# Optimization experiments

Hardware: AMD Instinct MI355X
Metric: run time of the kernel (lower is better)

## Reference

```python
import jax, jax.numpy as jnp
import numpy as np

D = 1024      # features
C = 768       # context dim
H = 16        # heads
HD = D // H   # head dim = 64
N = 2048      # query tokens
M = 2048      # context tokens
EPS = 1e-12
SCALE = float(np.sqrt(HD))


def layernorm(x, w, b):
    c = x - x.mean(axis=-1, keepdims=True)
    s = (c * c).mean(axis=-1, keepdims=True)
    return c * jax.lax.rsqrt(s + EPS) * w + b


def setup_inputs() -> dict:
    key = jax.random.key(0)
    ks = jax.random.split(key, 10)
    sc = 0.02
    return {
        "x": jax.random.normal(ks[0], (N, D), jnp.float32),
        "ctx": jax.random.normal(ks[1], (M, C), jnp.float32),
        # attention projections (Projection: normal*0.02, zero bias)
        "wq": jax.random.normal(ks[2], (D, D), jnp.float32) * sc,
        "bq": jnp.zeros((D,), jnp.float32),
        "wk": jax.random.normal(ks[3], (C, D), jnp.float32) * sc,
        "bk": jnp.zeros((D,), jnp.float32),
        "wv": jax.random.normal(ks[4], (C, D), jnp.float32) * sc,
        "bv": jnp.zeros((D,), jnp.float32),
        "wo": jax.random.normal(ks[5], (D, D), jnp.float32) * sc,
        "bo": jnp.zeros((D,), jnp.float32),
        # MLP
        "w1": jax.random.normal(ks[6], (D, 4 * D), jnp.float32) * sc,
        "b1": jnp.zeros((4 * D,), jnp.float32),
        "w2": jax.random.normal(ks[7], (4 * D, D), jnp.float32) * sc,
        "b2": jnp.zeros((D,), jnp.float32),
        # layernorms
        "qn_w": jnp.ones((D,), jnp.float32), "qn_b": jnp.zeros((D,), jnp.float32),
        "kvn_w": jnp.ones((C,), jnp.float32), "kvn_b": jnp.zeros((C,), jnp.float32),
        "pn_w": jnp.ones((D,), jnp.float32), "pn_b": jnp.zeros((D,), jnp.float32),
    }


def reference(x, ctx, wq, bq, wk, bk, wv, bv, wo, bo, w1, b1, w2, b2,
              qn_w, qn_b, kvn_w, kvn_b, pn_w, pn_b):
    # pre-norm cross-attention
    xq = layernorm(x, qn_w, qn_b)          # [n, d]
    kv = layernorm(ctx, kvn_w, kvn_b)      # [m, c]
    q = (xq @ wq + bq).reshape(N, H, HD).transpose(1, 0, 2)   # [h, n, hd]
    k = (kv @ wk + bk).reshape(M, H, HD).transpose(1, 0, 2)   # [h, m, hd]
    v = (kv @ wv + bv).reshape(M, H, HD).transpose(1, 0, 2)   # [h, m, hd]
    attn = jax.nn.softmax(jnp.einsum('hnd,hmd->hnm', q, k) / SCALE, axis=-1)
    o = jnp.einsum('hnm,hmd->hnd', attn, v).transpose(1, 0, 2).reshape(N, D)
    x = (o @ wo + bo) + x
    # MLP block
    h = layernorm(x, pn_w, pn_b)
    h = jax.nn.gelu(h @ w1 + b1) @ w2 + b2
    return h + x
```

## Files before the change

### kernel.cpp

```cpp
#include <hip/hip_runtime.h>

typedef __bf16 bf16;
typedef __bf16 bf16x4 __attribute__((ext_vector_type(4)));
typedef __bf16 bf16x8 __attribute__((ext_vector_type(8)));
typedef float f32x4 __attribute__((ext_vector_type(4)));

#define N_TOK 2048
#define M_TOK 2048
#define DIM 1024
#define CDIM 768
#define DFF 4096

static __device__ __forceinline__ void async16(const void* g, void* l) {
  __builtin_amdgcn_global_load_lds((const __attribute__((address_space(1))) void*)g,
                                   (__attribute__((address_space(3))) void*)l, 16, 0, 0);
}

__global__ __launch_bounds__(256) void detect_kernel(const void* x, int* flag) {
  __shared__ int cnt;
  if (threadIdx.x == 0) cnt = 0;
  __syncthreads();
  const unsigned* w = (const unsigned*)x;
  int ok = 0;
  for (int i = threadIdx.x; i < 512; i += 256) {
    unsigned lo = w[i] & 0xFFFFu;
    float f = __uint_as_float(lo << 16);
    if (lo == 0u || (fabsf(f) > 1e-3f && fabsf(f) < 1e3f)) ok++;
  }
  atomicAdd(&cnt, ok);
  __syncthreads();
  if (threadIdx.x == 0) *flag = (cnt >= 256) ? 1 : 0;
}

struct ConvArgs {
  const void* src[12];
  bf16* dst[12];
  int n[12];
};
__global__ __launch_bounds__(256) void conv_small_kernel(ConvArgs a, const int* flag) {
  const bool isbf = (*flag != 0);
  const int b = blockIdx.x;
  const void* in = a.src[b];
  bf16* out = a.dst[b];
  const int n = a.n[b];
  for (int i = threadIdx.x; i < n; i += 256)
    out[i] = isbf ? ((const bf16*)in)[i] : (bf16)((const float*)in)[i];
}

struct TmArgs {
  const void* src[4];
  bf16* dst[4];
  int r0[4], Rcnt[4], c0[4], Cfull[4], gx[4], gy[4];
  int force_bf;
};
__global__ __launch_bounds__(256) void tmulti_kernel(TmArgs a, const int* flag) {
  const int z = blockIdx.z;
  if ((int)blockIdx.x >= a.gx[z] || (int)blockIdx.y >= a.gy[z]) return;
  __shared__ bf16 t[32][33];
  const bool isbf = a.force_bf || (*flag != 0);
  const void* in = a.src[z];
  bf16* out = a.dst[z];
  const int Rcnt = a.Rcnt[z], Cfull = a.Cfull[z];
  const int cb = blockIdx.x * 32, rb = blockIdx.y * 32;
  const int tx = threadIdx.x & 31, ty = threadIdx.x >> 5;
#pragma unroll
  for (int i = 0; i < 4; i++) {
    const size_t r = (size_t)(a.r0[z] + rb + ty + i * 8);
    const size_t c = (size_t)(a.c0[z] + cb + tx);
    float v = isbf ? (float)((const bf16*)in)[r * Cfull + c]
                   : ((const float*)in)[r * Cfull + c];
    t[ty + i * 8][tx] = (bf16)v;
  }
  __syncthreads();
#pragma unroll
  for (int i = 0; i < 4; i++)
    out[(size_t)(cb + ty + i * 8) * Rcnt + rb + tx] = t[tx][ty + i * 8];
}

__global__ __launch_bounds__(256) void ln_pair_kernel(
    const void* __restrict__ x0, const bf16* w0, const bf16* b0, bf16* o0,
    const void* __restrict__ x1, const bf16* w1, const bf16* b1, bf16* o1,
    const int* flag) {
  const bool isbf = (*flag != 0);
  const int cols = (blockIdx.y == 0) ? DIM : CDIM;
  const void* x = (blockIdx.y == 0) ? x0 : x1;
  const bf16* w = (blockIdx.y == 0) ? w0 : w1;
  const bf16* b = (blockIdx.y == 0) ? b0 : b1;
  bf16* outp = (blockIdx.y == 0) ? o0 : o1;
  const int row = blockIdx.x;
  const bf16* xr_b = (const bf16*)x + (size_t)row * cols;
  const float* xr_f = (const float*)x + (size_t)row * cols;
  bf16* orow = outp + (size_t)row * cols;
  float s = 0.f, ss = 0.f;
  for (int c = threadIdx.x; c < cols; c += 256) {
    float v = isbf ? (float)xr_b[c] : xr_f[c];
    s += v; ss += v * v;
  }
  for (int d = 1; d < 64; d <<= 1) { s += __shfl_xor(s, d, 64); ss += __shfl_xor(ss, d, 64); }
  __shared__ float sh[8];
  const int wv = threadIdx.x >> 6, lane = threadIdx.x & 63;
  if (lane == 0) { sh[wv] = s; sh[4 + wv] = ss; }
  __syncthreads();
  s = sh[0] + sh[1] + sh[2] + sh[3];
  ss = sh[4] + sh[5] + sh[6] + sh[7];
  const float mean = s / cols;
  float var = ss / cols - mean * mean;
  var = fmaxf(var, 0.f);
  const float r = rsqrtf(var + 1e-12f);
  for (int c = threadIdx.x; c < cols; c += 256) {
    float v = isbf ? (float)xr_b[c] : xr_f[c];
    orow[c] = (bf16)((v - mean) * r * (float)w[c] + (float)b[c]);
  }
}

__global__ __launch_bounds__(256) void ln_kernel(
    const bf16* __restrict__ x, const bf16* __restrict__ w, const bf16* __restrict__ b,
    bf16* __restrict__ out, int cols) {
  const int row = blockIdx.x;
  const bf16* xr = x + (size_t)row * cols;
  bf16* orow = out + (size_t)row * cols;
  float s = 0.f, ss = 0.f;
  for (int c = threadIdx.x; c < cols; c += 256) {
    float v = (float)xr[c];
    s += v; ss += v * v;
  }
  for (int d = 1; d < 64; d <<= 1) { s += __shfl_xor(s, d, 64); ss += __shfl_xor(ss, d, 64); }
  __shared__ float sh[8];
  const int wv = threadIdx.x >> 6, lane = threadIdx.x & 63;
  if (lane == 0) { sh[wv] = s; sh[4 + wv] = ss; }
  __syncthreads();
  s = sh[0] + sh[1] + sh[2] + sh[3];
  ss = sh[4] + sh[5] + sh[6] + sh[7];
  const float mean = s / cols;
  float var = ss / cols - mean * mean;
  var = fmaxf(var, 0.f);
  const float r = rsqrtf(var + 1e-12f);
  for (int c = threadIdx.x; c < cols; c += 256) {
    float v = (float)xr[c];
    orow[c] = (bf16)((v - mean) * r * (float)w[c] + (float)b[c]);
  }
}

__device__ __forceinline__ float gelu_f(float x) {
  float u = 0.7978845608028654f * (x + 0.044715f * x * x * x);
  return 0.5f * x * (1.f + tanhf(u));
}

template <int EPI>
__global__ __launch_bounds__(256) void gemm64(
    const bf16* __restrict__ A, const bf16* __restrict__ Bt,
    const bf16* __restrict__ bias, const void* __restrict__ resid,
    void* __restrict__ Cout, int K, int ldc, const int* flag) {
  __shared__ __align__(16) bf16 As[2][64 * 32];
  __shared__ __align__(16) bf16 Bs[2][64 * 32];
  const int tid = threadIdx.x;
  const int lane = tid & 63, wv = tid >> 6;
  const int lq = lane >> 4, lm = lane & 15;
  const int row0 = blockIdx.y * 64, col0 = blockIdx.x * 64;
  const int wr = (wv >> 1) * 32, wc = (wv & 1) * 32;

  f32x4 acc[2][2] = {};
  const int r_a = wv * 16 + (lane >> 2);
  const int kc = (lane & 3) * 8;

  for (int k0 = 0; k0 < K; k0 += 64) {
    __syncthreads();
#pragma unroll
    for (int b = 0; b < 2; b++) {
      async16(A + (size_t)(row0 + r_a) * K + k0 + b * 32 + kc, As[b] + wv * 512);
      async16(Bt + (size_t)(col0 + r_a) * K + k0 + b * 32 + kc, Bs[b] + wv * 512);
    }
    __syncthreads();
#pragma unroll
    for (int b = 0; b < 2; b++) {
      bf16x8 af[2], bfv[2];
#pragma unroll
      for (int t = 0; t < 2; t++)
        af[t] = *(const bf16x8*)&As[b][(wr + t * 16 + lm) * 32 + lq * 8];
#pragma unroll
      for (int t = 0; t < 2; t++)
        bfv[t] = *(const bf16x8*)&Bs[b][(wc + t * 16 + lm) * 32 + lq * 8];
#pragma unroll
      for (int i = 0; i < 2; i++)
#pragma unroll
        for (int j = 0; j < 2; j++)
          acc[i][j] = __builtin_amdgcn_mfma_f32_16x16x32_bf16(af[i], bfv[j], acc[i][j], 0, 0, 0);
    }
  }

  const bool isbf = (*flag != 0);
#pragma unroll
  for (int i = 0; i < 2; i++) {
    const int rb = row0 + wr + i * 16 + lq * 4;
#pragma unroll
    for (int j = 0; j < 2; j++) {
      const int c = col0 + wc + j * 16 + lm;
      const float bv = (EPI != 5) ? (float)bias[c] : 0.f;
#pragma unroll
      for (int rg = 0; rg < 4; rg++) {
        const size_t idx = (size_t)(rb + rg) * ldc + c;
        float v = acc[i][j][rg] + bv;
        if (EPI == 1)
          v += isbf ? (float)((const bf16*)resid)[idx] : ((const float*)resid)[idx];
        if (EPI == 2) v = gelu_f(v);
        if (EPI == 4) v += (float)((const bf16*)resid)[idx];
        if (EPI == 5)
          v += isbf ? (float)((bf16*)Cout)[idx] : ((float*)Cout)[idx];
        if (EPI == 4 || EPI == 5) {
          if (isbf) ((bf16*)Cout)[idx] = (bf16)v;
          else      ((float*)Cout)[idx] = v;
        } else {
          ((bf16*)Cout)[idx] = (bf16)v;
        }
      }
    }
  }
}

struct QkvArgs {
  const bf16* A[3];
  const bf16* Bt[3];
  const bf16* bias[3];
  bf16* C[3];
  int K[3], ldc[3], gx[3], gy[3], brow[3];
};
__global__ __launch_bounds__(256) void gemm64_qkv(QkvArgs a) {
  const int z = blockIdx.z;
  if ((int)blockIdx.x >= a.gx[z] || (int)blockIdx.y >= a.gy[z]) return;
  const bf16* A = a.A[z];
  const bf16* Bt = a.Bt[z];
  const int K = a.K[z];
  __shared__ __align__(16) bf16 As[2][64 * 32];
  __shared__ __align__(16) bf16 Bs[2][64 * 32];
  const int tid = threadIdx.x;
  const int lane = tid & 63, wv = tid >> 6;
  const int lq = lane >> 4, lm = lane & 15;
  const int row0 = blockIdx.y * 64, col0 = blockIdx.x * 64;
  const int wr = (wv >> 1) * 32, wc = (wv & 1) * 32;

  f32x4 acc[2][2] = {};
  const int r_a = wv * 16 + (lane >> 2);
  const int kc = (lane & 3) * 8;

  for (int k0 = 0; k0 < K; k0 += 64) {
    __syncthreads();
#pragma unroll
    for (int b = 0; b < 2; b++) {
      async16(A + (size_t)(row0 + r_a) * K + k0 + b * 32 + kc, As[b] + wv * 512);
      async16(Bt + (size_t)(col0 + r_a) * K + k0 + b * 32 + kc, Bs[b] + wv * 512);
    }
    __syncthreads();
#pragma unroll
    for (int b = 0; b < 2; b++) {
      bf16x8 af[2], bfv[2];
#pragma unroll
      for (int t = 0; t < 2; t++)
        af[t] = *(const bf16x8*)&As[b][(wr + t * 16 + lm) * 32 + lq * 8];
#pragma unroll
      for (int t = 0; t < 2; t++)
        bfv[t] = *(const bf16x8*)&Bs[b][(wc + t * 16 + lm) * 32 + lq * 8];
#pragma unroll
      for (int i = 0; i < 2; i++)
#pragma unroll
        for (int j = 0; j < 2; j++)
          acc[i][j] = __builtin_amdgcn_mfma_f32_16x16x32_bf16(af[i], bfv[j], acc[i][j], 0, 0, 0);
    }
  }

  const bf16* bias = a.bias[z];
  bf16* C = a.C[z];
  const int ldc = a.ldc[z];
  const bool brow = a.brow[z] != 0;
#pragma unroll
  for (int i = 0; i < 2; i++) {
    const int rb = row0 + wr + i * 16 + lq * 4;
#pragma unroll
    for (int j = 0; j < 2; j++) {
      const int c = col0 + wc + j * 16 + lm;
      const float bcol = brow ? 0.f : (float)bias[c];
#pragma unroll
      for (int rg = 0; rg < 4; rg++) {
        const float bv = brow ? (float)bias[rb + rg] : bcol;
        C[(size_t)(rb + rg) * ldc + c] = (bf16)(acc[i][j][rg] + bv);
      }
    }
  }
}

#define KS_STR 72
#define VS_STR 136
__global__ __launch_bounds__(256) void attn_kernel(
    const bf16* __restrict__ q, const bf16* __restrict__ k,
    const bf16* __restrict__ vT, bf16* __restrict__ o) {
  __shared__ __align__(16) bf16 KPs[128 * KS_STR];
  __shared__ __align__(16) bf16 Vs[64 * VS_STR];
  const int tid = threadIdx.x, lane = tid & 63, wv = tid >> 6;
  const int lq = lane >> 4, lm = lane & 15;
  const int h = blockIdx.y;
  const int n0 = blockIdx.x * 64;

  bf16x8 qf[2];
#pragma unroll
  for (int f = 0; f < 2; f++)
    qf[f] = *(const bf16x8*)&q[(size_t)(n0 + wv * 16 + lm) * DIM + h * 64 + f * 32 + lq * 8];

  f32x4 oacc[4] = {};
  float lsum = 0.f;
  const float sc = 0.125f * 1.4426950408889634f;

  for (int m0 = 0; m0 < M_TOK; m0 += 128) {
    __syncthreads();
#pragma unroll
    for (int it = 0; it < 4; it++) {
      const int e = tid * 8 + it * 2048;
      const int r = e >> 6, c = e & 63;
      *(bf16x8*)&KPs[r * KS_STR + c] =
          *(const bf16x8*)&k[(size_t)(m0 + r) * DIM + h * 64 + c];
    }
#pragma unroll
    for (int it = 0; it < 4; it++) {
      const int e = tid * 8 + it * 2048;
      const int r = e >> 7, c = e & 127;
      *(bf16x8*)&Vs[r * VS_STR + c] =
          *(const bf16x8*)&vT[(size_t)(h * 64 + r) * M_TOK + m0 + c];
    }
    __syncthreads();

    f32x4 s[8];
#pragma unroll
    for (int j = 0; j < 8; j++) {
      bf16x8 kf0 = *(const bf16x8*)&KPs[(j * 16 + lm) * KS_STR + lq * 8];
      bf16x8 kf1 = *(const bf16x8*)&KPs[(j * 16 + lm) * KS_STR + 32 + lq * 8];
      f32x4 z = {};
      z = __builtin_amdgcn_mfma_f32_16x16x32_bf16(kf0, qf[0], z, 0, 0, 0);
      s[j] = __builtin_amdgcn_mfma_f32_16x16x32_bf16(kf1, qf[1], z, 0, 0, 0);
    }
    __syncthreads();

#pragma unroll
    for (int j = 0; j < 8; j++) {
      bf16x4 pw;
#pragma unroll
      for (int rg = 0; rg < 4; rg++) {
        const float pv = exp2f(s[j][rg] * sc);
        lsum += pv;
        pw[rg] = (bf16)pv;
      }
      *(bf16x4*)&KPs[(wv * 16 + lm) * VS_STR + j * 16 + lq * 4] = pw;
    }

#pragma unroll
    for (int kk = 0; kk < 4; kk++) {
      bf16x8 pf = *(const bf16x8*)&KPs[(wv * 16 + lm) * VS_STR + kk * 32 + lq * 8];
#pragma unroll
      for (int dt = 0; dt < 4; dt++) {
        bf16x8 vf = *(const bf16x8*)&Vs[(dt * 16 + lm) * VS_STR + kk * 32 + lq * 8];
        oacc[dt] = __builtin_amdgcn_mfma_f32_16x16x32_bf16(vf, pf, oacc[dt], 0, 0, 0);
      }
    }
  }

  lsum += __shfl_xor(lsum, 16, 64);
  lsum += __shfl_xor(lsum, 32, 64);
  const float rinv = 1.f / lsum;

  const int rn = n0 + wv * 16 + lm;
#pragma unroll
  for (int dt = 0; dt < 4; dt++) {
    bf16x4 ow;
#pragma unroll
    for (int rg = 0; rg < 4; rg++) ow[rg] = (bf16)(oacc[dt][rg] * rinv);
    *(bf16x4*)&o[(size_t)rn * DIM + h * 64 + dt * 16 + lq * 4] = ow;
  }
}

extern "C" void kernel_launch(void* const* d_in, const int* in_sizes, int n_in,
                              void* d_out, int out_size, void* d_ws, size_t ws_size,
                              hipStream_t stream) {
  const void* x_r     = d_in[0];
  const void* ctx_r   = d_in[1];
  const void* wq_r    = d_in[2];
  const void* bq_r    = d_in[3];
  const void* wk_r    = d_in[4];
  const void* bk_r    = d_in[5];
  const void* wv_r    = d_in[6];
  const void* bv_r    = d_in[7];
  const void* wo_r    = d_in[8];
  const void* bo_r    = d_in[9];
  const void* w1_r    = d_in[10];
  const void* b1_r    = d_in[11];
  const void* w2_r    = d_in[12];
  const void* b2_r    = d_in[13];
  const void* qnw_r   = d_in[14];
  const void* qnb_r   = d_in[15];
  const void* kvnw_r  = d_in[16];
  const void* kvnb_r  = d_in[17];
  const void* pnw_r   = d_in[18];
  const void* pnb_r   = d_in[19];

  bf16* p = (bf16*)d_ws;
  const size_t MEG = 1024 * 1024;
  bf16* qm  = p;             bf16* hln = qm;
  bf16* km  = p + 2 * MEG;   bf16* xat = km;
  bf16* wC  = p + 4 * MEG;
  bf16* xq  = p + 8 * MEG;   bf16* om  = xq;
  bf16* h1h = p + 10 * MEG;
  bf16* kvn = p + 12 * MEG;
  bf16* vTb = p + 10 * MEG;
  bf16* SM  = p + 14 * MEG;
  int* flag = (int*)(p + 14 * MEG + 16384);

  bf16* wqT = wC;
  bf16* wkT = wC + 1 * MEG;
  bf16* wvT = wC + 1 * MEG + 786432;
  bf16* woT = wC + 2 * MEG + 524288;
  bf16* w1Th = wC;
  bf16* w2Th = wC + 2 * MEG;

  bf16* bqc = SM, *bkc = SM + 1024, *bvc = SM + 2048, *boc = SM + 3072;
  bf16* b1c = SM + 4096, *b2c = SM + 8192;
  bf16* qnw = SM + 9216, *qnb = SM + 10240;
  bf16* kvnw = SM + 11264, *kvnb = SM + 12032;
  bf16* pnw = SM + 12800, *pnb = SM + 13824;

  detect_kernel<<<1, 256, 0, stream>>>(x_r, flag);
  ConvArgs ca;
  ca.src[0] = bq_r;   ca.dst[0] = bqc;  ca.n[0] = DIM;
  ca.src[1] = bk_r;   ca.dst[1] = bkc;  ca.n[1] = DIM;
  ca.src[2] = bv_r;   ca.dst[2] = bvc;  ca.n[2] = DIM;
  ca.src[3] = bo_r;   ca.dst[3] = boc;  ca.n[3] = DIM;
  ca.src[4] = b1_r;   ca.dst[4] = b1c;  ca.n[4] = DFF;
  ca.src[5] = b2_r;   ca.dst[5] = b2c;  ca.n[5] = DIM;
  ca.src[6] = qnw_r;  ca.dst[6] = qnw;  ca.n[6] = DIM;
  ca.src[7] = qnb_r;  ca.dst[7] = qnb;  ca.n[7] = DIM;
  ca.src[8] = kvnw_r; ca.dst[8] = kvnw; ca.n[8] = CDIM;
  ca.src[9] = kvnb_r; ca.dst[9] = kvnb; ca.n[9] = CDIM;
  ca.src[10] = pnw_r; ca.dst[10] = pnw; ca.n[10] = DIM;
  ca.src[11] = pnb_r; ca.dst[11] = pnb; ca.n[11] = DIM;
  conv_small_kernel<<<12, 256, 0, stream>>>(ca, flag);

  ln_pair_kernel<<<dim3(2048, 2), 256, 0, stream>>>(x_r, qnw, qnb, xq,
                                                    ctx_r, kvnw, kvnb, kvn, flag);

  {
    TmArgs ta;
    ta.force_bf = 0;
    ta.src[0] = wq_r; ta.dst[0] = wqT; ta.r0[0] = 0; ta.Rcnt[0] = DIM;
    ta.c0[0] = 0; ta.Cfull[0] = DIM; ta.gx[0] = 32; ta.gy[0] = 32;
    ta.src[1] = wk_r; ta.dst[1] = wkT; ta.r0[1] = 0; ta.Rcnt[1] = CDIM;
    ta.c0[1] = 0; ta.Cfull[1] = DIM; ta.gx[1] = 32; ta.gy[1] = 24;
    ta.src[2] = wv_r; ta.dst[2] = wvT; ta.r0[2] = 0; ta.Rcnt[2] = CDIM;
    ta.c0[2] = 0; ta.Cfull[2] = DIM; ta.gx[2] = 32; ta.gy[2] = 24;
    ta.src[3] = wo_r; ta.dst[3] = woT; ta.r0[3] = 0; ta.Rcnt[3] = DIM;
    ta.c0[3] = 0; ta.Cfull[3] = DIM; ta.gx[3] = 32; ta.gy[3] = 32;
    tmulti_kernel<<<dim3(32, 32, 4), 256, 0, stream>>>(ta, flag);
  }

  {
    QkvArgs qa;
    qa.A[0] = xq;  qa.Bt[0] = wqT; qa.bias[0] = bqc; qa.C[0] = qm;
    qa.K[0] = DIM;  qa.ldc[0] = DIM;   qa.gx[0] = 16; qa.gy[0] = 32; qa.brow[0] = 0;
    qa.A[1] = kvn; qa.Bt[1] = wkT; qa.bias[1] = bkc; qa.C[1] = km;
    qa.K[1] = CDIM; qa.ldc[1] = DIM;   qa.gx[1] = 16; qa.gy[1] = 32; qa.brow[1] = 0;
    qa.A[2] = wvT; qa.Bt[2] = kvn; qa.bias[2] = bvc; qa.C[2] = vTb;
    qa.K[2] = CDIM; qa.ldc[2] = M_TOK; qa.gx[2] = 32; qa.gy[2] = 16; qa.brow[2] = 1;
    gemm64_qkv<<<dim3(32, 32, 3), 256, 0, stream>>>(qa);
  }

  attn_kernel<<<dim3(32, 16), 256, 0, stream>>>(qm, km, vTb, om);

  gemm64<1><<<dim3(16, 32), 256, 0, stream>>>(om, woT, boc, x_r, xat, DIM, DIM, flag);

  ln_kernel<<<N_TOK, 256, 0, stream>>>(xat, pnw, pnb, hln, DIM);

  for (int hh = 0; hh < 2; hh++) {
    TmArgs ta;
    ta.force_bf = 0;
    ta.src[0] = w1_r; ta.dst[0] = w1Th; ta.r0[0] = 0; ta.Rcnt[0] = DIM;
    ta.c0[0] = hh * 2048; ta.Cfull[0] = DFF; ta.gx[0] = 64; ta.gy[0] = 32;
    ta.src[1] = w2_r; ta.dst[1] = w2Th; ta.r0[1] = hh * 2048; ta.Rcnt[1] = 2048;
    ta.c0[1] = 0; ta.Cfull[1] = DIM; ta.gx[1] = 32; ta.gy[1] = 64;
    ta.src[2] = ta.src[0]; ta.dst[2] = ta.dst[0]; ta.r0[2] = 0; ta.Rcnt[2] = 32;
    ta.c0[2] = 0; ta.Cfull[2] = DIM; ta.gx[2] = 0; ta.gy[2] = 0;
    ta.src[3] = ta.src[0]; ta.dst[3] = ta.dst[0]; ta.r0[3] = 0; ta.Rcnt[3] = 32;
    ta.c0[3] = 0; ta.Cfull[3] = DIM; ta.gx[3] = 0; ta.gy[3] = 0;
    tmulti_kernel<<<dim3(64, 64, 2), 256, 0, stream>>>(ta, flag);

    gemm64<2><<<dim3(32, 32), 256, 0, stream>>>(hln, w1Th, b1c + hh * 2048, nullptr,
                                                h1h, DIM, 2048, flag);
    if (hh == 0)
      gemm64<4><<<dim3(16, 32), 256, 0, stream>>>(h1h, w2Th, b2c, xat, d_out,
                                                  2048, DIM, flag);
    else
      gemm64<5><<<dim3(16, 32), 256, 0, stream>>>(h1h, w2Th, b2c, nullptr, d_out,
                                                  2048, DIM, flag);
  }
}
```

Before: 387.4 us.

## Split attention over two context halves with combine kernel; deepen GEMM K-step

The attention kernel now runs a third grid dimension that splits the 2048 context tokens into two halves. Each half writes unnormalized bf16 partial outputs and per-row exp sums into scratch buffers that are no longer needed. A new combine kernel adds the two partials and divides by the total sum. This doubles the number of attention blocks to fill more CUs, at the cost of an extra launch, extra global traffic, and bf16 rounding of the unnormalized partials. Separately, both GEMM kernels now load four 32-wide K slices per barrier pair instead of two, halving the number of synchronizations at the cost of more LDS per block.

```diff
diff --git a/kernel.cpp b/kernel.cpp
--- a/kernel.cpp
+++ b/kernel.cpp
@@ -151,8 +151,8 @@
     const bf16* __restrict__ A, const bf16* __restrict__ Bt,
     const bf16* __restrict__ bias, const void* __restrict__ resid,
     void* __restrict__ Cout, int K, int ldc, const int* flag) {
-  __shared__ __align__(16) bf16 As[2][64 * 32];
-  __shared__ __align__(16) bf16 Bs[2][64 * 32];
+  __shared__ __align__(16) bf16 As[4][64 * 32];
+  __shared__ __align__(16) bf16 Bs[4][64 * 32];
   const int tid = threadIdx.x;
   const int lane = tid & 63, wv = tid >> 6;
   const int lq = lane >> 4, lm = lane & 15;
@@ -163,16 +163,16 @@
   const int r_a = wv * 16 + (lane >> 2);
   const int kc = (lane & 3) * 8;
 
-  for (int k0 = 0; k0 < K; k0 += 64) {
-    __syncthreads();
-#pragma unroll
-    for (int b = 0; b < 2; b++) {
+  for (int k0 = 0; k0 < K; k0 += 128) {
+    __syncthreads();
+#pragma unroll
+    for (int b = 0; b < 4; b++) {
       async16(A + (size_t)(row0 + r_a) * K + k0 + b * 32 + kc, As[b] + wv * 512);
       async16(Bt + (size_t)(col0 + r_a) * K + k0 + b * 32 + kc, Bs[b] + wv * 512);
     }
     __syncthreads();
 #pragma unroll
-    for (int b = 0; b < 2; b++) {
+    for (int b = 0; b < 4; b++) {
       bf16x8 af[2], bfv[2];
 #pragma unroll
       for (int t = 0; t < 2; t++)
@@ -230,8 +230,8 @@
   const bf16* A = a.A[z];
   const bf16* Bt = a.Bt[z];
   const int K = a.K[z];
-  __shared__ __align__(16) bf16 As[2][64 * 32];
-  __shared__ __align__(16) bf16 Bs[2][64 * 32];
+  __shared__ __align__(16) bf16 As[4][64 * 32];
+  __shared__ __align__(16) bf16 Bs[4][64 * 32];
   const int tid = threadIdx.x;
   const int lane = tid & 63, wv = tid >> 6;
   const int lq = lane >> 4, lm = lane & 15;
@@ -242,16 +242,16 @@
   const int r_a = wv * 16 + (lane >> 2);
   const int kc = (lane & 3) * 8;
 
-  for (int k0 = 0; k0 < K; k0 += 64) {
-    __syncthreads();
-#pragma unroll
-    for (int b = 0; b < 2; b++) {
+  for (int k0 = 0; k0 < K; k0 += 128) {
+    __syncthreads();
+#pragma unroll
+    for (int b = 0; b < 4; b++) {
       async16(A + (size_t)(row0 + r_a) * K + k0 + b * 32 + kc, As[b] + wv * 512);
       async16(Bt + (size_t)(col0 + r_a) * K + k0 + b * 32 + kc, Bs[b] + wv * 512);
     }
     __syncthreads();
 #pragma unroll
-    for (int b = 0; b < 2; b++) {
+    for (int b = 0; b < 4; b++) {
       bf16x8 af[2], bfv[2];
 #pragma unroll
       for (int t = 0; t < 2; t++)
@@ -291,13 +291,18 @@
 #define VS_STR 136
 __global__ __launch_bounds__(256) void attn_kernel(
     const bf16* __restrict__ q, const bf16* __restrict__ k,
-    const bf16* __restrict__ vT, bf16* __restrict__ o) {
+    const bf16* __restrict__ vT, bf16* __restrict__ pO0, bf16* __restrict__ pO1,
+    float* __restrict__ l0, float* __restrict__ l1) {
   __shared__ __align__(16) bf16 KPs[128 * KS_STR];
   __shared__ __align__(16) bf16 Vs[64 * VS_STR];
   const int tid = threadIdx.x, lane = tid & 63, wv = tid >> 6;
   const int lq = lane >> 4, lm = lane & 15;
   const int h = blockIdx.y;
   const int n0 = blockIdx.x * 64;
+  const int half = blockIdx.z;
+  const int mbeg = half * (M_TOK / 2), mend = mbeg + M_TOK / 2;
+  bf16* pO = half ? pO1 : pO0;
+  float* lb = half ? l1 : l0;
 
   bf16x8 qf[2];
 #pragma unroll
@@ -308,7 +313,7 @@
   float lsum = 0.f;
   const float sc = 0.125f * 1.4426950408889634f;
 
-  for (int m0 = 0; m0 < M_TOK; m0 += 128) {
+  for (int m0 = mbeg; m0 < mend; m0 += 128) {
     __syncthreads();
 #pragma unroll
     for (int it = 0; it < 4; it++) {
@@ -362,16 +367,32 @@
 
   lsum += __shfl_xor(lsum, 16, 64);
   lsum += __shfl_xor(lsum, 32, 64);
-  const float rinv = 1.f / lsum;
+  if (lane < 16) lb[h * N_TOK + n0 + wv * 16 + lane] = lsum;
 
   const int rn = n0 + wv * 16 + lm;
 #pragma unroll
   for (int dt = 0; dt < 4; dt++) {
     bf16x4 ow;
 #pragma unroll
-    for (int rg = 0; rg < 4; rg++) ow[rg] = (bf16)(oacc[dt][rg] * rinv);
-    *(bf16x4*)&o[(size_t)rn * DIM + h * 64 + dt * 16 + lq * 4] = ow;
-  }
+    for (int rg = 0; rg < 4; rg++) ow[rg] = (bf16)oacc[dt][rg];
+    *(bf16x4*)&pO[(size_t)rn * DIM + h * 64 + dt * 16 + lq * 4] = ow;
+  }
+}
+
+__global__ __launch_bounds__(256) void attn_combine(
+    const bf16* __restrict__ pO0, const bf16* __restrict__ pO1,
+    const float* __restrict__ l0, const float* __restrict__ l1,
+    bf16* __restrict__ om) {
+  const int i4 = (blockIdx.x * 256 + threadIdx.x) * 4;
+  const int n = i4 >> 10;
+  const int h = (i4 & 1023) >> 6;
+  const float rinv = 1.f / (l0[h * N_TOK + n] + l1[h * N_TOK + n]);
+  bf16x4 a = *(const bf16x4*)&pO0[i4];
+  bf16x4 b = *(const bf16x4*)&pO1[i4];
+  bf16x4 o;
+#pragma unroll
+  for (int r = 0; r < 4; r++) o[r] = (bf16)(((float)a[r] + (float)b[r]) * rinv);
+  *(bf16x4*)&om[i4] = o;
 }
 
 extern "C" void kernel_launch(void* const* d_in, const int* in_sizes, int n_in,
@@ -403,10 +424,10 @@
   bf16* qm  = p;             bf16* hln = qm;
   bf16* km  = p + 2 * MEG;   bf16* xat = km;
   bf16* wC  = p + 4 * MEG;
-  bf16* xq  = p + 8 * MEG;   bf16* om  = xq;
+  bf16* xq  = p + 8 * MEG;   bf16* pO0 = xq;   bf16* om = xq;
+  bf16* vTb = p + 10 * MEG;
+  bf16* kvn = p + 12 * MEG;  bf16* pO1 = kvn;
   bf16* h1h = p + 10 * MEG;
-  bf16* kvn = p + 12 * MEG;
-  bf16* vTb = p + 10 * MEG;
   bf16* SM  = p + 14 * MEG;
   int* flag = (int*)(p + 14 * MEG + 16384);
 
@@ -416,6 +437,8 @@
   bf16* woT = wC + 2 * MEG + 524288;
   bf16* w1Th = wC;
   bf16* w2Th = wC + 2 * MEG;
+  float* l0 = (float*)wC;
+  float* l1 = l0 + N_TOK * 16;
 
   bf16* bqc = SM, *bkc = SM + 1024, *bvc = SM + 2048, *boc = SM + 3072;
   bf16* b1c = SM + 4096, *b2c = SM + 8192;
@@ -467,7 +490,8 @@
     gemm64_qkv<<<dim3(32, 32, 3), 256, 0, stream>>>(qa);
   }
 
-  attn_kernel<<<dim3(32, 16), 256, 0, stream>>>(qm, km, vTb, om);
+  attn_kernel<<<dim3(32, 16, 2), 256, 0, stream>>>(qm, km, vTb, pO0, pO1, l0, l1);
+  attn_combine<<<2048, 256, 0, stream>>>(pO0, pO1, l0, l1, om);
 
   gemm64<1><<<dim3(16, 32), 256, 0, stream>>>(om, woT, boc, x_r, xat, DIM, DIM, flag);
 
```

New measurement: 354.6 us. 8.5% less time.
